# Kernel optimization log

Measured on AMD Instinct MI355X. Metric: run time of the kernel, lower is better.

The kernel has to match this reference:

```python
import jax, jax.numpy as jnp
import numpy as np

B, S, H, NH, HD = 64, 200, 1024, 16, 64
MAX_LEN = 200
FF = 4 * H


def _ln(x, g, b):
    m = x.mean(-1, keepdims=True)
    v = ((x - m) ** 2).mean(-1, keepdims=True)
    return (x - m) / jnp.sqrt(v + 1e-5) * g + b


def setup_inputs() -> dict:
    key = jax.random.key(0)
    k = jax.random.split(key, 24)
    s = 0.02
    f32 = jnp.float32
    return {
        "x": jax.random.normal(k[0], (B, S, H), f32),
        "time": jax.random.uniform(k[1], (B, S, 1), dtype=f32),
        "wq": jax.random.normal(k[2], (H, H), f32) * s,
        "bq": jnp.zeros((H,), f32),
        "wk": jax.random.normal(k[3], (H, H), f32) * s,
        "bk": jnp.zeros((H,), f32),
        "wv": jax.random.normal(k[4], (H, H), f32) * s,
        "bv": jnp.zeros((H,), f32),
        "wo": jax.random.normal(k[5], (H, H), f32) * s,
        "bo": jnp.zeros((H,), f32),
        "wt": jax.random.normal(k[6], (1, H), f32) * s,
        "bt": jnp.zeros((H,), f32),
        "pos_embed": jax.random.normal(k[7], (2 * MAX_LEN - 1, HD), f32) * s,
        "g1": jnp.ones((H,), f32),
        "be1": jnp.zeros((H,), f32),
        "g2": jnp.ones((H,), f32),
        "be2": jnp.zeros((H,), f32),
        "w1": jax.random.normal(k[8], (H, FF), f32) * s,
        "bf1": jnp.zeros((FF,), f32),
        "w2": jax.random.normal(k[9], (FF, H), f32) * s,
        "bf2": jnp.zeros((H,), f32),
    }


def reference(x, time, wq, bq, wk, bk, wv, bv, wo, bo, wt, bt, pos_embed,
              g1, be1, g2, be2, w1, bf1, w2, bf2):
    b, s, hs = x.shape
    residual = x
    h = _ln(x, g1, be1)
    h = h + time @ wt + bt  # time embedding added post-LN
    q = (h @ wq + bq).reshape(b, s, NH, HD).transpose(0, 2, 1, 3)  # [b,h,s,d]
    k = (h @ wk + bk).reshape(b, s, NH, HD).transpose(0, 2, 1, 3)
    v = (h @ wv + bv).reshape(b, s, NH, HD).transpose(0, 2, 1, 3)
    scale = np.float32(1.0 / np.sqrt(HD))
    scores = jnp.einsum('bhqd,bhkd->bhqk', q, k) * scale
    # gathered relative position bias (NOT scaled, added after scaling)
    idx = jnp.arange(s)
    rel = jnp.clip(idx[:, None] - idx[None, :] + (MAX_LEN - 1), 0, 2 * MAX_LEN - 2)
    rel_emb = pos_embed[rel]  # [s, s, HD]
    scores = scores + jnp.einsum('bhqd,qkd->bhqk', q, rel_emb)
    causal_mask = jnp.triu(jnp.ones((s, s), bool), 1)
    scores = jnp.where(causal_mask, jnp.float32(-1e9), scores)
    attn = jax.nn.softmax(scores, axis=-1)
    ctx = jnp.einsum('bhqk,bhkd->bhqd', attn, v)
    ctx = ctx.transpose(0, 2, 1, 3).reshape(b, s, hs)
    out = ctx @ wo + bo + residual
    res2 = out
    h2 = _ln(out, g2, be2)
    ff = jax.nn.gelu(h2 @ w1 + bf1, approximate=False) @ w2 + bf2
    return ff + res2
```

## Files before the change

kernel.cpp:

```cpp
#include <hip/hip_runtime.h>

#define B_SZ   64
#define S_LEN  200
#define H_DIM  1024
#define NHEAD  16
#define HDIM   64
#define FF_DIM 4096
#define NROWS  (B_SZ * S_LEN)

typedef __bf16 bf16x8 __attribute__((ext_vector_type(8)));
typedef float  f32x4  __attribute__((ext_vector_type(4)));

#define GLOBAL_AS __attribute__((address_space(1)))
#define LDS_AS    __attribute__((address_space(3)))

__device__ __forceinline__ void g2lds16(const void* g, void* l) {
  __builtin_amdgcn_global_load_lds((const GLOBAL_AS void*)g, (LDS_AS void*)l, 16, 0, 0);
}

__device__ __forceinline__ float b2f(ushort u) {
  return __uint_as_float(((unsigned int)u) << 16);
}
__device__ __forceinline__ ushort f2b(float f) {
  unsigned int u = __float_as_uint(f);
  u += 0x7fffu + ((u >> 16) & 1u);
  return (ushort)(u >> 16);
}
__device__ __forceinline__ bf16x8 ld_g16(const ushort* p) {
  union { uint4 u; bf16x8 v; } r; r.u = *(const uint4*)p; return r.v;
}
__device__ __forceinline__ bf16x8 ld_lds8x2(const ushort* p) {
  union { uint2 u[2]; bf16x8 v; } r;
  r.u[0] = *(const uint2*)p;
  r.u[1] = *(const uint2*)(p + 4);
  return r.v;
}

__global__ __launch_bounds__(256) void prep_kernel(
    const float* __restrict__ wq, const float* __restrict__ wk,
    const float* __restrict__ wv, const float* __restrict__ wo,
    const float* __restrict__ w1, const float* __restrict__ w2,
    const float* __restrict__ bq, const float* __restrict__ bk,
    const float* __restrict__ bv_, const float* __restrict__ pos,
    ushort* __restrict__ wqkv_t, ushort* __restrict__ wo_t,
    ushort* __restrict__ w1_t, ushort* __restrict__ w2_t,
    float* __restrict__ bqkv, ushort* __restrict__ pos_bf) {
  int id = blockIdx.x;
  if (id < 12288) {
    const float* src; ushort* dst; int K, N, tile;
    if (id < 4096) {
      K = 1024; N = 1024; tile = id & 1023;
      int m = id >> 10;
      src = (m == 0) ? wq : (m == 1) ? wk : (m == 2) ? wv : wo;
      dst = (m == 3) ? wo_t : wqkv_t + (size_t)m * 1024 * 1024;
    } else if (id < 8192) {
      K = 1024; N = 4096; tile = id - 4096; src = w1; dst = w1_t;
    } else {
      K = 4096; N = 1024; tile = id - 8192; src = w2; dst = w2_t;
    }
    int nx = N >> 5;
    int nb = (tile % nx) * 32, kb = (tile / nx) * 32;
    __shared__ float t32[32][33];
    int tx = threadIdx.x & 31, ty = threadIdx.x >> 5;
#pragma unroll
    for (int i = 0; i < 4; ++i)
      t32[ty + i * 8][tx] = src[(size_t)(kb + ty + i * 8) * N + nb + tx];
    __syncthreads();
#pragma unroll
    for (int i = 0; i < 4; ++i)
      dst[(size_t)(nb + ty + i * 8) * K + kb + tx] = f2b(t32[tx][ty + i * 8]);
  } else {
    int t = threadIdx.x;
    for (int i = t; i < 1024; i += 256) {
      bqkv[i] = bq[i]; bqkv[1024 + i] = bk[i]; bqkv[2048 + i] = bv_[i];
    }
    for (int i = t; i < 12800; i += 256)
      pos_bf[i] = f2b(pos[(size_t)199 * 64 + i]);
  }
}

template <int HAS_TIME>
__global__ __launch_bounds__(256) void ln_kernel(
    const float* __restrict__ x, const float* __restrict__ g, const float* __restrict__ be,
    const float* __restrict__ tv, const float* __restrict__ wt, const float* __restrict__ bt,
    ushort* __restrict__ out) {
  int wave = threadIdx.x >> 6, lane = threadIdx.x & 63;
  int r = blockIdx.x * 4 + wave;
  const float4* xr = (const float4*)(x + (size_t)r * H_DIM);
  float4 xv[4];
  float s = 0.f, s2 = 0.f;
#pragma unroll
  for (int k = 0; k < 4; ++k) {
    xv[k] = xr[lane + 64 * k];
    s  += xv[k].x + xv[k].y + xv[k].z + xv[k].w;
    s2 += xv[k].x * xv[k].x + xv[k].y * xv[k].y + xv[k].z * xv[k].z + xv[k].w * xv[k].w;
  }
#pragma unroll
  for (int off = 32; off; off >>= 1) {
    s  += __shfl_xor(s, off);
    s2 += __shfl_xor(s2, off);
  }
  float m    = s * (1.0f / H_DIM);
  float var  = s2 * (1.0f / H_DIM) - m * m;
  float rstd = rsqrtf(var + 1e-5f);
  float tval = HAS_TIME ? tv[r] : 0.0f;
  ushort4* orow = (ushort4*)(out + (size_t)r * H_DIM);
#pragma unroll
  for (int k = 0; k < 4; ++k) {
    float4 gv = ((const float4*)g)[lane + 64 * k];
    float4 bv = ((const float4*)be)[lane + 64 * k];
    float v0 = (xv[k].x - m) * rstd * gv.x + bv.x;
    float v1 = (xv[k].y - m) * rstd * gv.y + bv.y;
    float v2 = (xv[k].z - m) * rstd * gv.z + bv.z;
    float v3 = (xv[k].w - m) * rstd * gv.w + bv.w;
    if (HAS_TIME) {
      float4 wv = ((const float4*)wt)[lane + 64 * k];
      float4 btv = ((const float4*)bt)[lane + 64 * k];
      v0 += tval * wv.x + btv.x;
      v1 += tval * wv.y + btv.y;
      v2 += tval * wv.z + btv.z;
      v3 += tval * wv.w + btv.w;
    }
    ushort4 o;
    o.x = f2b(v0); o.y = f2b(v1); o.z = f2b(v2); o.w = f2b(v3);
    orow[lane + 64 * k] = o;
  }
}

template <int EPI>
__global__ __launch_bounds__(256) void gemm_bt(
    const ushort* __restrict__ A, const ushort* __restrict__ Bt,
    const float* __restrict__ bias, void* __restrict__ Cv,
    const float* __restrict__ resid, int M, int N, int K) {
  __shared__ __align__(16) ushort As[2 * 128 * 32];
  __shared__ __align__(16) ushort Bs[2 * 128 * 32];
  int t = threadIdx.x;
  int lane = t & 63, wave = t >> 6;
  int wm = wave >> 1, wn = wave & 1;
  int r15 = lane & 15, quad = lane >> 4;
  int nwg = gridDim.x * gridDim.y;
  int bid = blockIdx.y * gridDim.x + blockIdx.x;
  int swz = (bid & 7) * (nwg >> 3) + (bid >> 3);
  int bx = swz % gridDim.x, by = swz / gridDim.x;
  size_t row0 = (size_t)by * 128;
  size_t col0 = (size_t)bx * 128;

  int srow = (lane >> 2), scol = (lane & 3) * 8;
  const ushort* ga0 = A  + (row0 + wave * 32 +      srow) * K + scol;
  const ushort* ga1 = A  + (row0 + wave * 32 + 16 + srow) * K + scol;
  const ushort* gb0 = Bt + (col0 + wave * 32 +      srow) * K + scol;
  const ushort* gb1 = Bt + (col0 + wave * 32 + 16 + srow) * K + scol;
  ushort* la0 = As + (wave * 32) * 32;
  ushort* la1 = As + (wave * 32 + 16) * 32;
  ushort* lb0 = Bs + (wave * 32) * 32;
  ushort* lb1 = Bs + (wave * 32 + 16) * 32;

  f32x4 acc[4][4] = {};

  for (int k0 = 0; k0 < K; k0 += 64) {
#pragma unroll
    for (int kh = 0; kh < 2; ++kh) {
      int go = k0 + kh * 32, lo = kh * 4096;
      g2lds16(ga0 + go, la0 + lo);
      g2lds16(ga1 + go, la1 + lo);
      g2lds16(gb0 + go, lb0 + lo);
      g2lds16(gb1 + go, lb1 + lo);
    }
    __syncthreads();
#pragma unroll
    for (int kh = 0; kh < 2; ++kh) {
      bf16x8 af[4], bfr[4];
#pragma unroll
      for (int i = 0; i < 4; ++i)
        af[i] = *(const bf16x8*)&As[kh * 4096 + (wm * 64 + i * 16 + r15) * 32 + quad * 8];
#pragma unroll
      for (int j = 0; j < 4; ++j)
        bfr[j] = *(const bf16x8*)&Bs[kh * 4096 + (wn * 64 + j * 16 + r15) * 32 + quad * 8];
#pragma unroll
      for (int i = 0; i < 4; ++i)
#pragma unroll
        for (int j = 0; j < 4; ++j)
          acc[i][j] = __builtin_amdgcn_mfma_f32_16x16x32_bf16(af[i], bfr[j], acc[i][j], 0, 0, 0);
    }
    __syncthreads();
  }

  int mbase = (int)row0 + wm * 64;
  int nbase = (int)col0 + wn * 64;
  float bb[4];
#pragma unroll
  for (int j = 0; j < 4; ++j) bb[j] = bias[nbase + j * 16 + r15];
#pragma unroll
  for (int i = 0; i < 4; ++i) {
#pragma unroll
    for (int ii = 0; ii < 4; ++ii) {
      int row = mbase + i * 16 + quad * 4 + ii;
      size_t rb = (size_t)row * N + nbase + r15;
#pragma unroll
      for (int j = 0; j < 4; ++j) {
        size_t idx = rb + j * 16;
        float v = acc[i][j][ii] + bb[j];
        if constexpr (EPI == 0) {
          ((ushort*)Cv)[idx] = f2b(v);
        } else if constexpr (EPI == 1) {
          float gl = 0.5f * v * (1.0f + erff(v * 0.70710678118f));
          ((ushort*)Cv)[idx] = f2b(gl);
        } else {
          ((float*)Cv)[idx] = v + resid[idx];
        }
      }
    }
  }
}

template <int IB>
__device__ __forceinline__ void mfma_blk(f32x4 (&acc)[8][4],
                                         const bf16x8 (&af)[4], const bf16x8 (&bfr)[4]) {
#pragma unroll
  for (int i = 0; i < 4; ++i)
#pragma unroll
    for (int j = 0; j < 4; ++j)
      acc[IB + i][j] =
          __builtin_amdgcn_mfma_f32_16x16x32_bf16(af[i], bfr[j], acc[IB + i][j], 0, 0, 0);
}

__device__ __forceinline__ bf16x8 rdfrag(const ushort* plane, int r, int quad) {
  return *(const bf16x8*)(plane + r * 32 + ((quad ^ ((r >> 1) & 3)) << 3));
}

__device__ __forceinline__ void read_q0(bf16x8 (&af)[4], bf16x8 (&bfr)[4],
                                        const ushort* pA, const ushort* pB,
                                        int wn1, int r15, int quad) {
#pragma unroll
  for (int j = 0; j < 4; ++j) bfr[j] = rdfrag(pB, wn1 * 64 + j * 16 + r15, quad);
#pragma unroll
  for (int i = 0; i < 4; ++i) af[i] = rdfrag(pA, i * 16 + r15, quad);
}
__device__ __forceinline__ void read_q1(bf16x8 (&af)[4], const ushort* pA,
                                        int r15, int quad) {
#pragma unroll
  for (int i = 0; i < 4; ++i) af[i] = rdfrag(pA, 64 + i * 16 + r15, quad);
}

#define VMW8() asm volatile("s_waitcnt vmcnt(8)" ::: "memory")
#define VMW4() asm volatile("s_waitcnt vmcnt(4)" ::: "memory")
#define VMW0() asm volatile("s_waitcnt vmcnt(0)" ::: "memory")
#define BARX() __builtin_amdgcn_s_barrier()
#define PRIO1() __builtin_amdgcn_s_setprio(1)
#define PRIO0() __builtin_amdgcn_s_setprio(0)

template <int EPI>
__global__ __launch_bounds__(512) void gemm256(
    const ushort* __restrict__ A, const ushort* __restrict__ Bt,
    const float* __restrict__ bias, void* __restrict__ Cv,
    const float* __restrict__ resid, int M, int N, int K) {
  __shared__ __align__(16) ushort lds[2][2][2][2][4096];
  const int t = threadIdx.x;
  const int lane = t & 63, wave = t >> 6;
  const int wm = wave >> 2;
  const int wn = wave & 3;
  const int wn1 = wn & 1;
  const int bh = wn >> 1;
  const int r15 = lane & 15, quad = lane >> 4;
  int nwg = gridDim.x * gridDim.y;
  int bid = blockIdx.y * gridDim.x + blockIdx.x;
  int swz = (bid & 7) * (nwg >> 3) + (bid >> 3);
  int bx = swz % gridDim.x, by = swz / gridDim.x;
  const size_t row0 = (size_t)by * 256;
  const size_t col0 = (size_t)bx * 256;

  const int gwA = wave & 3;
  const int gwB = ((wave >> 1) & 2) | (wave & 1);

  const ushort *gA0, *gA1, *gB0, *gB1;
  {
    int p0 = gwA * 128 + lane;
    int p1 = p0 + 64;
    int ra0 = p0 >> 2, sa0 = (p0 & 3) ^ ((p0 >> 3) & 3);
    int ra1 = p1 >> 2, sa1 = (p1 & 3) ^ ((p1 >> 3) & 3);
    gA0 = A + (row0 + wm * 128 + ra0) * K + sa0 * 8;
    gA1 = A + (row0 + wm * 128 + ra1) * K + sa1 * 8;
    int q0 = gwB * 128 + lane;
    int q1 = q0 + 64;
    int rb0 = q0 >> 2, sb0 = (q0 & 3) ^ ((q0 >> 3) & 3);
    int rb1 = q1 >> 2, sb1 = (q1 & 3) ^ ((q1 >> 3) & 3);
    gB0 = Bt + (col0 + bh * 128 + rb0) * K + sb0 * 8;
    gB1 = Bt + (col0 + bh * 128 + rb1) * K + sb1 * 8;
  }
  const int ldsA0 = gwA * 1024, ldsA1 = gwA * 1024 + 512;
  const int ldsB0 = gwB * 1024, ldsB1 = gwB * 1024 + 512;

#define STAGE_A(nb_, skh_, kof_)                                        \
  do {                                                                  \
    g2lds16(gA0 + (kof_) + (skh_) * 32, &lds[nb_][0][wm][skh_][ldsA0]); \
    g2lds16(gA1 + (kof_) + (skh_) * 32, &lds[nb_][0][wm][skh_][ldsA1]); \
  } while (0)
#define STAGE_B(nb_, skh_, kof_)                                        \
  do {                                                                  \
    g2lds16(gB0 + (kof_) + (skh_) * 32, &lds[nb_][1][bh][skh_][ldsB0]); \
    g2lds16(gB1 + (kof_) + (skh_) * 32, &lds[nb_][1][bh][skh_][ldsB1]); \
  } while (0)
#define PAP(b_, k_) (&lds[b_][0][wm][k_][0])
#define PBP(b_, k_) (&lds[b_][1][bh][k_][0])

  f32x4 acc[8][4] = {};

  STAGE_A(0, 0, 0);
  STAGE_B(0, 0, 0);
  STAGE_A(0, 1, 0);
  STAGE_B(0, 1, 0);
  STAGE_A(1, 0, 64);
  STAGE_B(1, 0, 64);
  VMW8();
  BARX();

#define ITER_BODY(LAST_, ka_)                                                  \
  {                                                                            \
    bf16x8 af[4], bfr[4];                                                      \
                                                          \
    read_q0(af, bfr, PAP(0, 0), PBP(0, 0), wn1, r15, quad);                    \
    STAGE_A(1, 1, (ka_) + 64);                                                 \
    BARX(); PRIO1(); mfma_blk<0>(acc, af, bfr); PRIO0(); BARX();               \
                                                          \
    read_q1(af, PAP(0, 0), r15, quad);                                         \
    STAGE_B(1, 1, (ka_) + 64);                                                 \
    BARX(); PRIO1(); mfma_blk<4>(acc, af, bfr); PRIO0();                       \
    VMW8(); BARX();                                                            \
                                                          \
    read_q0(af, bfr, PAP(0, 1), PBP(0, 1), wn1, r15, quad);                    \
    if (!(LAST_)) STAGE_A(0, 0, (ka_) + 128);                                  \
    BARX(); PRIO1(); mfma_blk<0>(acc, af, bfr); PRIO0(); BARX();               \
                                                          \
    read_q1(af, PAP(0, 1), r15, quad);                                         \
    if (!(LAST_)) STAGE_B(0, 0, (ka_) + 128);                                  \
    BARX(); PRIO1(); mfma_blk<4>(acc, af, bfr); PRIO0();                       \
    if (LAST_) { VMW4(); } else { VMW8(); }                                    \
    BARX();                                                                    \
                                                          \
    read_q0(af, bfr, PAP(1, 0), PBP(1, 0), wn1, r15, quad);                    \
    if (!(LAST_)) STAGE_A(0, 1, (ka_) + 128);                                  \
    BARX(); PRIO1(); mfma_blk<0>(acc, af, bfr); PRIO0(); BARX();               \
                                                          \
    read_q1(af, PAP(1, 0), r15, quad);                                         \
    if (!(LAST_)) STAGE_B(0, 1, (ka_) + 128);                                  \
    BARX(); PRIO1(); mfma_blk<4>(acc, af, bfr); PRIO0();                       \
    if (LAST_) { VMW0(); } else { VMW8(); }                                    \
    BARX();                                                                    \
                                                          \
    read_q0(af, bfr, PAP(1, 1), PBP(1, 1), wn1, r15, quad);                    \
    if (!(LAST_)) STAGE_A(1, 0, (ka_) + 192);                                  \
    BARX(); PRIO1(); mfma_blk<0>(acc, af, bfr); PRIO0(); BARX();               \
                                                          \
    read_q1(af, PAP(1, 1), r15, quad);                                         \
    if (!(LAST_)) STAGE_B(1, 0, (ka_) + 192);                                  \
    BARX(); PRIO1(); mfma_blk<4>(acc, af, bfr); PRIO0();                       \
    if (!(LAST_)) { VMW8(); }                                                  \
    BARX();                                                                    \
  }

  const int NI = K >> 7;
  for (int it = 0; it < NI - 1; ++it) {
    ITER_BODY(0, it << 7);
  }
  ITER_BODY(1, (NI - 1) << 7);
#undef ITER_BODY

  int mbase = (int)row0 + wm * 128;
  int nbase = (int)col0 + wn * 64;
  float bb[4];
#pragma unroll
  for (int j = 0; j < 4; ++j) bb[j] = bias[nbase + j * 16 + r15];
#pragma unroll
  for (int i = 0; i < 8; ++i) {
#pragma unroll
    for (int ii = 0; ii < 4; ++ii) {
      int row = mbase + i * 16 + quad * 4 + ii;
      size_t rb = (size_t)row * N + nbase + r15;
#pragma unroll
      for (int j = 0; j < 4; ++j) {
        size_t idx = rb + j * 16;
        float v = acc[i][j][ii] + bb[j];
        if constexpr (EPI == 0) {
          ((ushort*)Cv)[idx] = f2b(v);
        } else if constexpr (EPI == 1) {
          float gl = 0.5f * v * (1.0f + erff(v * 0.70710678118f));
          ((ushort*)Cv)[idx] = f2b(gl);
        } else {
          ((float*)Cv)[idx] = v + resid[idx];
        }
      }
    }
  }
#undef STAGE_A
#undef STAGE_B
#undef PAP
#undef PBP
}

#define PW_STRIDE 228
__global__ __launch_bounds__(256) void attn_kernel(
    const ushort* __restrict__ qkv, const ushort* __restrict__ pos_bf,
    ushort* __restrict__ ctx) {
  int bh = blockIdx.x;
  int b = bh >> 4, h = bh & 15;
  __shared__ ushort Vt[64][PW_STRIDE];
  __shared__ ushort Pw[4][16][PW_STRIDE];
  int t = threadIdx.x, lane = t & 63, wave = t >> 6;
  int r15 = lane & 15, quad = lane >> 4;
  const size_t base = ((size_t)b * S_LEN) * 3072 + (size_t)h * 64;

  for (int i = t; i < 64 * 28; i += 256) Vt[i / 28][200 + (i % 28)] = 0;
  for (int i = t; i < 800; i += 256) {
    int kp = i >> 3, d0 = (i & 7) * 8;
    int k = kp * 2;
    union { uint4 v; ushort u[8]; } r0, r1;
    r0.v = *(const uint4*)&qkv[base + (size_t)k * 3072 + 2048 + d0];
    r1.v = *(const uint4*)&qkv[base + (size_t)(k + 1) * 3072 + 2048 + d0];
#pragma unroll
    for (int j = 0; j < 8; ++j) {
      ushort2 w2; w2.x = r0.u[j]; w2.y = r1.u[j];
      *(ushort2*)&Vt[d0 + j][k] = w2;
    }
  }
  __syncthreads();

  for (int idx = wave; idx < 13; idx += 4) {
    int qt = (int)((0x3421058769ABCull >> (4 * idx)) & 0xFull);
    int q0 = qt * 16;
    int qrow = q0 + r15; if (qrow > 199) qrow = 199;
    const ushort* qp = qkv + base + (size_t)qrow * 3072;
    bf16x8 aq0 = ld_g16(qp + quad * 8);
    bf16x8 aq1 = ld_g16(qp + 32 + quad * 8);
    ushort* pw = &Pw[wave][0][0];

#pragma unroll
    for (int dt = 0; dt < 13; ++dt) {
      if (dt > qt) continue;
      int prow = dt * 16 + r15; if (prow > 199) prow = 199;
      const ushort* pp = pos_bf + (size_t)prow * 64;
      bf16x8 p0 = ld_g16(pp + quad * 8);
      bf16x8 p1 = ld_g16(pp + 32 + quad * 8);
      f32x4 tt = {};
      tt = __builtin_amdgcn_mfma_f32_16x16x32_bf16(aq0, p0, tt, 0, 0, 0);
      tt = __builtin_amdgcn_mfma_f32_16x16x32_bf16(aq1, p1, tt, 0, 0, 0);
#pragma unroll
      for (int ii = 0; ii < 4; ++ii)
        pw[(quad * 4 + ii) * PW_STRIDE + dt * 16 + r15] = f2b(tt[ii]);
    }

    f32x4 sreg[13];
    float rowmax[4] = {-3.0e38f, -3.0e38f, -3.0e38f, -3.0e38f};
#pragma unroll
    for (int kt = 0; kt < 13; ++kt) {
      if (kt > qt) continue;
      int krow = kt * 16 + r15; if (krow > 199) krow = 199;
      const ushort* kp = qkv + base + (size_t)krow * 3072 + 1024;
      bf16x8 k0 = ld_g16(kp + quad * 8);
      bf16x8 k1 = ld_g16(kp + 32 + quad * 8);
      f32x4 s = {};
      s = __builtin_amdgcn_mfma_f32_16x16x32_bf16(aq0, k0, s, 0, 0, 0);
      s = __builtin_amdgcn_mfma_f32_16x16x32_bf16(aq1, k1, s, 0, 0, 0);
      int k = kt * 16 + r15;
#pragma unroll
      for (int ii = 0; ii < 4; ++ii) {
        int q = q0 + quad * 4 + ii;
        float v;
        if (k <= q) {
          v = s[ii] * 0.125f + b2f(pw[(quad * 4 + ii) * PW_STRIDE + (q - k)]);
        } else {
          v = -1.0e30f;
        }
        s[ii] = v;
        rowmax[ii] = fmaxf(rowmax[ii], v);
      }
      sreg[kt] = s;
    }
#pragma unroll
    for (int off = 8; off; off >>= 1)
#pragma unroll
      for (int ii = 0; ii < 4; ++ii)
        rowmax[ii] = fmaxf(rowmax[ii], __shfl_xor(rowmax[ii], off));

    float rsum[4] = {0.f, 0.f, 0.f, 0.f};
#pragma unroll
    for (int kt = 0; kt < 13; ++kt) {
      if (kt > qt) continue;
#pragma unroll
      for (int ii = 0; ii < 4; ++ii) {
        float e = __expf(sreg[kt][ii] - rowmax[ii]);
        rsum[ii] += e;
        pw[(quad * 4 + ii) * PW_STRIDE + kt * 16 + r15] = f2b(e);
      }
    }
    if ((qt & 1) == 0) {
#pragma unroll
      for (int ii = 0; ii < 4; ++ii)
        pw[(quad * 4 + ii) * PW_STRIDE + (qt + 1) * 16 + r15] = 0;
    }
#pragma unroll
    for (int off = 8; off; off >>= 1)
#pragma unroll
      for (int ii = 0; ii < 4; ++ii)
        rsum[ii] += __shfl_xor(rsum[ii], off);
    float rinv[4];
#pragma unroll
    for (int ii = 0; ii < 4; ++ii) rinv[ii] = 1.0f / rsum[ii];

    int nk = (q0 + 15) / 32 + 1;
    f32x4 acc[4] = {};
#pragma unroll
    for (int k32 = 0; k32 < 7; ++k32) {
      if (k32 >= nk) continue;
      bf16x8 ap = ld_lds8x2(&pw[r15 * PW_STRIDE + k32 * 32 + quad * 8]);
#pragma unroll
      for (int n = 0; n < 4; ++n) {
        bf16x8 bv = ld_lds8x2(&Vt[n * 16 + r15][k32 * 32 + quad * 8]);
        acc[n] = __builtin_amdgcn_mfma_f32_16x16x32_bf16(ap, bv, acc[n], 0, 0, 0);
      }
    }
#pragma unroll
    for (int n = 0; n < 4; ++n)
#pragma unroll
      for (int ii = 0; ii < 4; ++ii) {
        int q = q0 + quad * 4 + ii;
        if (q < S_LEN)
          ctx[((size_t)(b * S_LEN + q)) * H_DIM + h * 64 + n * 16 + r15] =
              f2b(acc[n][ii] * rinv[ii]);
      }
  }
}

extern "C" void kernel_launch(void* const* d_in, const int* in_sizes, int n_in,
                              void* d_out, int out_size, void* d_ws, size_t ws_size,
                              hipStream_t stream) {
  (void)in_sizes; (void)n_in; (void)out_size; (void)ws_size;
  const float* x    = (const float*)d_in[0];
  const float* timev= (const float*)d_in[1];
  const float* wq   = (const float*)d_in[2];
  const float* bq   = (const float*)d_in[3];
  const float* wk   = (const float*)d_in[4];
  const float* bk   = (const float*)d_in[5];
  const float* wv   = (const float*)d_in[6];
  const float* bv   = (const float*)d_in[7];
  const float* wo   = (const float*)d_in[8];
  const float* bo   = (const float*)d_in[9];
  const float* wt   = (const float*)d_in[10];
  const float* bt   = (const float*)d_in[11];
  const float* pos  = (const float*)d_in[12];
  const float* g1   = (const float*)d_in[13];
  const float* be1  = (const float*)d_in[14];
  const float* g2   = (const float*)d_in[15];
  const float* be2  = (const float*)d_in[16];
  const float* w1   = (const float*)d_in[17];
  const float* bf1  = (const float*)d_in[18];
  const float* w2   = (const float*)d_in[19];
  const float* bf2  = (const float*)d_in[20];

  char* ws = (char*)d_ws;
  ushort* wqkv_t = (ushort*)ws;   ws += (size_t)3072 * 1024 * 2;
  ushort* wo_t   = (ushort*)ws;   ws += (size_t)1024 * 1024 * 2;
  ushort* w1_t   = (ushort*)ws;   ws += (size_t)4096 * 1024 * 2;
  ushort* w2_t   = (ushort*)ws;   ws += (size_t)1024 * 4096 * 2;
  float*  bqkv   = (float*)ws;    ws += (size_t)16384;
  ushort* pos_bf = (ushort*)ws;   ws += (size_t)200 * 64 * 2;
  char* r1 = ws;                  ws += (size_t)NROWS * 3072 * 2;
  ushort* qkv  = (ushort*)r1;
  ushort* h2   = (ushort*)r1;
  ushort* gbuf = (ushort*)(r1 + (size_t)NROWS * H_DIM * 2);
  char* r2 = ws;                  ws += (size_t)NROWS * 1024 * 2;
  ushort* hbf = (ushort*)r2;
  ushort* ctx = (ushort*)r2;
  float* res2 = (float*)d_out;

  prep_kernel<<<12289, 256, 0, stream>>>(wq, wk, wv, wo, w1, w2, bq, bk, bv, pos,
                                         wqkv_t, wo_t, w1_t, w2_t, bqkv, pos_bf);

  ln_kernel<1><<<NROWS / 4, 256, 0, stream>>>(x, g1, be1, timev, wt, bt, hbf);

  gemm256<0><<<dim3(12, 50), 512, 0, stream>>>(hbf, wqkv_t, bqkv, qkv, nullptr,
                                               NROWS, 3072, 1024);
  attn_kernel<<<B_SZ * NHEAD, 256, 0, stream>>>(qkv, pos_bf, ctx);

  gemm256<2><<<dim3(4, 50), 512, 0, stream>>>(ctx, wo_t, bo, res2, x,
                                              NROWS, 1024, 1024);
  ln_kernel<0><<<NROWS / 4, 256, 0, stream>>>(res2, g2, be2, nullptr, nullptr, nullptr, h2);

  for (int c = 0; c < 2; ++c) {
    size_t ro = (size_t)c * 6400;
    gemm256<1><<<dim3(16, 25), 512, 0, stream>>>(h2 + ro * 1024, w1_t, bf1, gbuf, nullptr,
                                                 6400, 4096, 1024);
    gemm_bt<2><<<dim3(8, 50), 256, 0, stream>>>(gbuf, w2_t, bf2, (float*)d_out + ro * 1024,
                                                res2 + ro * 1024, 6400, 1024, 4096);
  }
}
```

Measured before the change: 773.1 us.

## Fuse first LayerNorm into prep kernel and run unchunked FFN when workspace allows

Folds the first LayerNorm into the weight-prep launch as extra blocks, removing one kernel launch. When the workspace is large enough, buffers are re-planned with aliasing so the FFN can run over all 12800 rows in one pass. That path uses the 256-tile gemm256 for the second FFN GEMM instead of two chunked gemm_bt launches. The cost is a larger workspace requirement and in-place residual accumulation into the output buffer. The code falls back to the old chunked schedule when the workspace is too small.

```diff
diff --git a/kernel.cpp b/kernel.cpp
--- a/kernel.cpp
+++ b/kernel.cpp
@@ -36,56 +36,12 @@
   return r.v;
 }
 
-__global__ __launch_bounds__(256) void prep_kernel(
-    const float* __restrict__ wq, const float* __restrict__ wk,
-    const float* __restrict__ wv, const float* __restrict__ wo,
-    const float* __restrict__ w1, const float* __restrict__ w2,
-    const float* __restrict__ bq, const float* __restrict__ bk,
-    const float* __restrict__ bv_, const float* __restrict__ pos,
-    ushort* __restrict__ wqkv_t, ushort* __restrict__ wo_t,
-    ushort* __restrict__ w1_t, ushort* __restrict__ w2_t,
-    float* __restrict__ bqkv, ushort* __restrict__ pos_bf) {
-  int id = blockIdx.x;
-  if (id < 12288) {
-    const float* src; ushort* dst; int K, N, tile;
-    if (id < 4096) {
-      K = 1024; N = 1024; tile = id & 1023;
-      int m = id >> 10;
-      src = (m == 0) ? wq : (m == 1) ? wk : (m == 2) ? wv : wo;
-      dst = (m == 3) ? wo_t : wqkv_t + (size_t)m * 1024 * 1024;
-    } else if (id < 8192) {
-      K = 1024; N = 4096; tile = id - 4096; src = w1; dst = w1_t;
-    } else {
-      K = 4096; N = 1024; tile = id - 8192; src = w2; dst = w2_t;
-    }
-    int nx = N >> 5;
-    int nb = (tile % nx) * 32, kb = (tile / nx) * 32;
-    __shared__ float t32[32][33];
-    int tx = threadIdx.x & 31, ty = threadIdx.x >> 5;
-#pragma unroll
-    for (int i = 0; i < 4; ++i)
-      t32[ty + i * 8][tx] = src[(size_t)(kb + ty + i * 8) * N + nb + tx];
-    __syncthreads();
-#pragma unroll
-    for (int i = 0; i < 4; ++i)
-      dst[(size_t)(nb + ty + i * 8) * K + kb + tx] = f2b(t32[tx][ty + i * 8]);
-  } else {
-    int t = threadIdx.x;
-    for (int i = t; i < 1024; i += 256) {
-      bqkv[i] = bq[i]; bqkv[1024 + i] = bk[i]; bqkv[2048 + i] = bv_[i];
-    }
-    for (int i = t; i < 12800; i += 256)
-      pos_bf[i] = f2b(pos[(size_t)199 * 64 + i]);
-  }
-}
-
 template <int HAS_TIME>
-__global__ __launch_bounds__(256) void ln_kernel(
+__device__ __forceinline__ void ln_row(
+    int r, int lane,
     const float* __restrict__ x, const float* __restrict__ g, const float* __restrict__ be,
     const float* __restrict__ tv, const float* __restrict__ wt, const float* __restrict__ bt,
     ushort* __restrict__ out) {
-  int wave = threadIdx.x >> 6, lane = threadIdx.x & 63;
-  int r = blockIdx.x * 4 + wave;
   const float4* xr = (const float4*)(x + (size_t)r * H_DIM);
   float4 xv[4];
   float s = 0.f, s2 = 0.f;
@@ -125,6 +81,65 @@
     o.x = f2b(v0); o.y = f2b(v1); o.z = f2b(v2); o.w = f2b(v3);
     orow[lane + 64 * k] = o;
   }
+}
+
+__global__ __launch_bounds__(256) void prep_kernel(
+    const float* __restrict__ wq, const float* __restrict__ wk,
+    const float* __restrict__ wv, const float* __restrict__ wo,
+    const float* __restrict__ w1, const float* __restrict__ w2,
+    const float* __restrict__ bq, const float* __restrict__ bk,
+    const float* __restrict__ bv_, const float* __restrict__ pos,
+    ushort* __restrict__ wqkv_t, ushort* __restrict__ wo_t,
+    ushort* __restrict__ w1_t, ushort* __restrict__ w2_t,
+    float* __restrict__ bqkv, ushort* __restrict__ pos_bf,
+    const float* __restrict__ x, const float* __restrict__ g1,
+    const float* __restrict__ be1, const float* __restrict__ tv,
+    const float* __restrict__ wt, const float* __restrict__ bt,
+    ushort* __restrict__ hbf) {
+  int id = blockIdx.x;
+  if (id < 12288) {
+    const float* src; ushort* dst; int K, N, tile;
+    if (id < 4096) {
+      K = 1024; N = 1024; tile = id & 1023;
+      int m = id >> 10;
+      src = (m == 0) ? wq : (m == 1) ? wk : (m == 2) ? wv : wo;
+      dst = (m == 3) ? wo_t : wqkv_t + (size_t)m * 1024 * 1024;
+    } else if (id < 8192) {
+      K = 1024; N = 4096; tile = id - 4096; src = w1; dst = w1_t;
+    } else {
+      K = 4096; N = 1024; tile = id - 8192; src = w2; dst = w2_t;
+    }
+    int nx = N >> 5;
+    int nb = (tile % nx) * 32, kb = (tile / nx) * 32;
+    __shared__ float t32[32][33];
+    int tx = threadIdx.x & 31, ty = threadIdx.x >> 5;
+#pragma unroll
+    for (int i = 0; i < 4; ++i)
+      t32[ty + i * 8][tx] = src[(size_t)(kb + ty + i * 8) * N + nb + tx];
+    __syncthreads();
+#pragma unroll
+    for (int i = 0; i < 4; ++i)
+      dst[(size_t)(nb + ty + i * 8) * K + kb + tx] = f2b(t32[tx][ty + i * 8]);
+  } else if (id == 12288) {
+    int t = threadIdx.x;
+    for (int i = t; i < 1024; i += 256) {
+      bqkv[i] = bq[i]; bqkv[1024 + i] = bk[i]; bqkv[2048 + i] = bv_[i];
+    }
+    for (int i = t; i < 12800; i += 256)
+      pos_bf[i] = f2b(pos[(size_t)199 * 64 + i]);
+  } else {
+    int wave = threadIdx.x >> 6, lane = threadIdx.x & 63;
+    int r = (id - 12289) * 4 + wave;
+    ln_row<1>(r, lane, x, g1, be1, tv, wt, bt, hbf);
+  }
+}
+
+__global__ __launch_bounds__(256) void ln_kernel(
+    const float* __restrict__ x, const float* __restrict__ g, const float* __restrict__ be,
+    ushort* __restrict__ out) {
+  int wave = threadIdx.x >> 6, lane = threadIdx.x & 63;
+  int r = blockIdx.x * 4 + wave;
+  ln_row<0>(r, lane, x, g, be, nullptr, nullptr, nullptr, out);
 }
 
 template <int EPI>
@@ -533,7 +548,7 @@
 extern "C" void kernel_launch(void* const* d_in, const int* in_sizes, int n_in,
                               void* d_out, int out_size, void* d_ws, size_t ws_size,
                               hipStream_t stream) {
-  (void)in_sizes; (void)n_in; (void)out_size; (void)ws_size;
+  (void)in_sizes; (void)n_in; (void)out_size;
   const float* x    = (const float*)d_in[0];
   const float* timev= (const float*)d_in[1];
   const float* wq   = (const float*)d_in[2];
@@ -556,40 +571,75 @@
   const float* w2   = (const float*)d_in[19];
   const float* bf2  = (const float*)d_in[20];
 
-  char* ws = (char*)d_ws;
-  ushort* wqkv_t = (ushort*)ws;   ws += (size_t)3072 * 1024 * 2;
-  ushort* wo_t   = (ushort*)ws;   ws += (size_t)1024 * 1024 * 2;
-  ushort* w1_t   = (ushort*)ws;   ws += (size_t)4096 * 1024 * 2;
-  ushort* w2_t   = (ushort*)ws;   ws += (size_t)1024 * 4096 * 2;
-  float*  bqkv   = (float*)ws;    ws += (size_t)16384;
-  ushort* pos_bf = (ushort*)ws;   ws += (size_t)200 * 64 * 2;
-  char* r1 = ws;                  ws += (size_t)NROWS * 3072 * 2;
-  ushort* qkv  = (ushort*)r1;
-  ushort* h2   = (ushort*)r1;
-  ushort* gbuf = (ushort*)(r1 + (size_t)NROWS * H_DIM * 2);
-  char* r2 = ws;                  ws += (size_t)NROWS * 1024 * 2;
-  ushort* hbf = (ushort*)r2;
-  ushort* ctx = (ushort*)r2;
+  const size_t SZ_W1T  = (size_t)4096 * 1024 * 2;
+  const size_t SZ_W2T  = (size_t)1024 * 4096 * 2;
+  const size_t SZ_SM   = 65536;
+  const size_t SZ_D    = (size_t)NROWS * H_DIM * 2;
+  const size_t SZ_E    = (size_t)NROWS * FF_DIM * 2;
+  const size_t NEED_UN = SZ_W1T + SZ_W2T + SZ_SM + SZ_D + SZ_E;
+
   float* res2 = (float*)d_out;
 
-  prep_kernel<<<12289, 256, 0, stream>>>(wq, wk, wv, wo, w1, w2, bq, bk, bv, pos,
-                                         wqkv_t, wo_t, w1_t, w2_t, bqkv, pos_bf);
-
-  ln_kernel<1><<<NROWS / 4, 256, 0, stream>>>(x, g1, be1, timev, wt, bt, hbf);
-
-  gemm256<0><<<dim3(12, 50), 512, 0, stream>>>(hbf, wqkv_t, bqkv, qkv, nullptr,
-                                               NROWS, 3072, 1024);
-  attn_kernel<<<B_SZ * NHEAD, 256, 0, stream>>>(qkv, pos_bf, ctx);
-
-  gemm256<2><<<dim3(4, 50), 512, 0, stream>>>(ctx, wo_t, bo, res2, x,
-                                              NROWS, 1024, 1024);
-  ln_kernel<0><<<NROWS / 4, 256, 0, stream>>>(res2, g2, be2, nullptr, nullptr, nullptr, h2);
-
-  for (int c = 0; c < 2; ++c) {
-    size_t ro = (size_t)c * 6400;
-    gemm256<1><<<dim3(16, 25), 512, 0, stream>>>(h2 + ro * 1024, w1_t, bf1, gbuf, nullptr,
-                                                 6400, 4096, 1024);
-    gemm_bt<2><<<dim3(8, 50), 256, 0, stream>>>(gbuf, w2_t, bf2, (float*)d_out + ro * 1024,
-                                                res2 + ro * 1024, 6400, 1024, 4096);
-  }
-}
+  if (ws_size >= NEED_UN) {
+    char* ws = (char*)d_ws;
+    ushort* w1_t   = (ushort*)ws;  ws += SZ_W1T;
+    ushort* w2_t   = (ushort*)ws;  ws += SZ_W2T;
+    float*  bqkv   = (float*)ws;
+    ushort* pos_bf = (ushort*)(ws + 16384);  ws += SZ_SM;
+    char*   slotD  = ws;           ws += SZ_D;
+    char*   slotE  = ws;           ws += SZ_E;
+    ushort* wqkv_t = (ushort*)slotD;
+    ushort* wo_t   = (ushort*)(slotD + (size_t)3072 * 1024 * 2);
+    ushort* h2     = (ushort*)slotD;
+    ushort* hbf    = (ushort*)slotE;
+    ushort* qkv    = (ushort*)(slotE + SZ_D);
+    ushort* ctx    = (ushort*)slotE;
+    ushort* gbuf   = (ushort*)slotE;
+
+    prep_kernel<<<15489, 256, 0, stream>>>(wq, wk, wv, wo, w1, w2, bq, bk, bv, pos,
+                                           wqkv_t, wo_t, w1_t, w2_t, bqkv, pos_bf,
+                                           x, g1, be1, timev, wt, bt, hbf);
+    gemm256<0><<<dim3(12, 50), 512, 0, stream>>>(hbf, wqkv_t, bqkv, qkv, nullptr,
+                                                 NROWS, 3072, 1024);
+    attn_kernel<<<B_SZ * NHEAD, 256, 0, stream>>>(qkv, pos_bf, ctx);
+    gemm256<2><<<dim3(4, 50), 512, 0, stream>>>(ctx, wo_t, bo, res2, x,
+                                                NROWS, 1024, 1024);
+    ln_kernel<<<NROWS / 4, 256, 0, stream>>>(res2, g2, be2, h2);
+    gemm256<1><<<dim3(16, 50), 512, 0, stream>>>(h2, w1_t, bf1, gbuf, nullptr,
+                                                 NROWS, 4096, 1024);
+    gemm256<2><<<dim3(4, 50), 512, 0, stream>>>(gbuf, w2_t, bf2, res2, res2,
+                                                NROWS, 1024, 4096);
+  } else {
+    char* ws = (char*)d_ws;
+    ushort* wqkv_t = (ushort*)ws;   ws += (size_t)3072 * 1024 * 2;
+    ushort* wo_t   = (ushort*)ws;   ws += (size_t)1024 * 1024 * 2;
+    ushort* w1_t   = (ushort*)ws;   ws += SZ_W1T;
+    ushort* w2_t   = (ushort*)ws;   ws += SZ_W2T;
+    float*  bqkv   = (float*)ws;    ws += (size_t)16384;
+    ushort* pos_bf = (ushort*)ws;   ws += (size_t)200 * 64 * 2;
+    char* r1 = ws;                  ws += (size_t)NROWS * 3072 * 2;
+    ushort* qkv  = (ushort*)r1;
+    ushort* h2   = (ushort*)r1;
+    ushort* gbuf = (ushort*)(r1 + (size_t)NROWS * H_DIM * 2);
+    char* r2 = ws;                  ws += (size_t)NROWS * 1024 * 2;
+    ushort* hbf = (ushort*)r2;
+    ushort* ctx = (ushort*)r2;
+
+    prep_kernel<<<15489, 256, 0, stream>>>(wq, wk, wv, wo, w1, w2, bq, bk, bv, pos,
+                                           wqkv_t, wo_t, w1_t, w2_t, bqkv, pos_bf,
+                                           x, g1, be1, timev, wt, bt, hbf);
+    gemm256<0><<<dim3(12, 50), 512, 0, stream>>>(hbf, wqkv_t, bqkv, qkv, nullptr,
+                                                 NROWS, 3072, 1024);
+    attn_kernel<<<B_SZ * NHEAD, 256, 0, stream>>>(qkv, pos_bf, ctx);
+    gemm256<2><<<dim3(4, 50), 512, 0, stream>>>(ctx, wo_t, bo, res2, x,
+                                                NROWS, 1024, 1024);
+    ln_kernel<<<NROWS / 4, 256, 0, stream>>>(res2, g2, be2, h2);
+    for (int c = 0; c < 2; ++c) {
+      size_t ro = (size_t)c * 6400;
+      gemm256<1><<<dim3(16, 25), 512, 0, stream>>>(h2 + ro * 1024, w1_t, bf1, gbuf, nullptr,
+                                                   6400, 4096, 1024);
+      gemm_bt<2><<<dim3(8, 50), 256, 0, stream>>>(gbuf, w2_t, bf2, (float*)d_out + ro * 1024,
+                                                  res2 + ro * 1024, 6400, 1024, 4096);
+    }
+  }
+}
```

After: 682.8 us. -11.7%, faster.
